# Optimization experiments

Hardware: AMD Instinct MI355X
Metric: run time of the kernel (lower is better)

Reference implementation:

```python
import jax, jax.numpy as jnp
import numpy as np

N = 100000   # nodes
E = 1250000  # edges
G = 64       # graphs in batch
F_IN, H, NT, GT = 29, 64, 6, 4
L = 4        # num GCN layers


def setup_inputs() -> dict:
    key = jax.random.key(0)
    ks = jax.random.split(key, 14)
    s_in = 1.0 / np.sqrt(F_IN)
    s_h = 1.0 / np.sqrt(H)
    return {
        "x": jax.random.normal(ks[0], (N, F_IN), dtype=jnp.float32),
        "edge_index": jax.random.randint(ks[1], (2, E), 0, N, dtype=jnp.int64),
        "batch": jnp.sort(jax.random.randint(ks[2], (N,), 0, G, dtype=jnp.int64)),
        "encW": jax.random.uniform(ks[3], (F_IN, H), jnp.float32, -s_in, s_in),
        "encb": jax.random.uniform(ks[4], (H,), jnp.float32, -s_in, s_in),
        "convW": jax.random.uniform(ks[5], (L, H, H), jnp.float32, -s_h, s_h),
        "convb": jax.random.uniform(ks[6], (L, H), jnp.float32, -s_h, s_h),
        "nodeW": jax.random.uniform(ks[7], (H, NT), jnp.float32, -s_h, s_h),
        "nodeb": jax.random.uniform(ks[8], (NT,), jnp.float32, -s_h, s_h),
        "g1W": jax.random.uniform(ks[9], (H, H), jnp.float32, -s_h, s_h),
        "g1b": jax.random.uniform(ks[10], (H,), jnp.float32, -s_h, s_h),
        "g2W": jax.random.uniform(ks[11], (H, GT), jnp.float32, -s_h, s_h),
        "g2b": jax.random.uniform(ks[12], (GT,), jnp.float32, -s_h, s_h),
    }


def reference(x, edge_index, batch, encW, encb, convW, convb, nodeW, nodeb, g1W, g1b, g2W, g2b):
    # GCNConv with self-loops and symmetric normalization (PyG defaults)
    loop = jnp.arange(N, dtype=edge_index.dtype)
    row = jnp.concatenate([edge_index[0], loop])  # senders
    col = jnp.concatenate([edge_index[1], loop])  # receivers
    deg = jax.ops.segment_sum(jnp.ones_like(col, dtype=x.dtype), col, num_segments=N)
    dis = jnp.where(deg > 0, deg ** -0.5, 0.0)
    norm = (dis[row] * dis[col])[:, None]  # [E+N, 1]

    h = jax.nn.relu(x @ encW + encb)
    for i in range(L):
        hw = h @ convW[i]  # transform then propagate
        agg = jax.ops.segment_sum(hw[row] * norm, col, num_segments=N)
        h = jax.nn.relu(agg + convb[i])

    pred_node = h @ nodeW + nodeb

    counts = jax.ops.segment_sum(jnp.ones((N,), x.dtype), batch, num_segments=G)
    gemb = jax.ops.segment_sum(h, batch, num_segments=G) / jnp.maximum(counts, 1.0)[:, None]
    pred_global = jax.nn.relu(gemb @ g1W + g1b) @ g2W + g2b
    return (pred_node, pred_global)
```

## Files before the change

### kernel.cpp

```cpp
#include <hip/hip_runtime.h>
#include <hip/hip_fp16.h>

#define N_NODES 100000
#define N_EDGES 1250000
#define N_GRAPHS 64
#define F_INN 29
#define HD 64
#define NT 6
#define GT 4
#define NLAYERS 4
#define RECS_CAP 3000000
#define NBLK 1563
#define NBUK 782
#define HGRID 256
#define GB_BLOCKS 391
#define ENC_BLOCKS 6250
#define NH_BLOCKS 3125

typedef __attribute__((ext_vector_type(8))) _Float16 f16x8;
typedef __attribute__((ext_vector_type(4))) float f32x4;

__global__ void hist1_misc(const int* __restrict__ col, int* __restrict__ ghistT, int E,
                           const float* __restrict__ convW, uint4* __restrict__ wfrag,
                           __half* __restrict__ ht1, __half* __restrict__ ht2,
                           const int* __restrict__ batch, int* __restrict__ start) {
    __shared__ int lh[NBUK];
    int tid = threadIdx.x, b = blockIdx.x;
    if (b < HGRID) {
        for (int i = tid; i < NBUK; i += 256) lh[i] = 0;
        __syncthreads();
        for (int e = b * 256 + tid; e < E; e += HGRID * 256) atomicAdd(&lh[col[e] >> 7], 1);
        __syncthreads();
        for (int i = tid; i < NBUK; i += 256) ghistT[i * 256 + b] = lh[i];
    } else if (b < HGRID + 4) {
        int layer = b - HGRID;
        const float* W = convW + (size_t)layer * HD * HD;
        uint4* out = wfrag + (size_t)layer * 512;
        for (int s = tid; s < 512; s += 256) {
            int jt = s >> 7, ks = (s >> 6) & 1, l = s & 63;
            int j = jt * 16 + (l & 15);
            int k0 = ks * 32 + (l >> 4) * 8;
            __align__(16) __half hh[8];
            #pragma unroll
            for (int i = 0; i < 8; ++i) hh[i] = __float2half_rn(W[(size_t)(k0 + i) * HD + j]);
            out[s] = *reinterpret_cast<const uint4*>(hh);
        }
    } else if (b == HGRID + 4) {
        if (tid < HD) ht1[(size_t)N_NODES * HD + tid] = __float2half_rn(0.f);
        else if (tid < 2 * HD) ht2[(size_t)N_NODES * HD + (tid - HD)] = __float2half_rn(0.f);
    } else {
        int i = (b - HGRID - 5) * 256 + tid;
        if (i < N_NODES) {
            int bb = batch[i];
            if (i == 0) {
                for (int g = 0; g <= bb; ++g) start[g] = 0;
            } else {
                int pb = batch[i - 1];
                if (pb != bb) for (int g = pb + 1; g <= bb; ++g) start[g] = i;
            }
            if (i == N_NODES - 1) {
                for (int g = bb + 1; g <= N_GRAPHS; ++g) start[g] = N_NODES;
            }
        }
    }
}

__global__ void hist_colscan(int* __restrict__ ghistT, int* __restrict__ tot) {
    __shared__ int wsum[4];
    int k = blockIdx.x, tid = threadIdx.x;
    int v = ghistT[k * 256 + tid];
    int incl = v;
    int lane = tid & 63;
    #pragma unroll
    for (int off = 1; off < 64; off <<= 1) {
        int t = __shfl_up(incl, (unsigned)off, 64);
        if (lane >= off) incl += t;
    }
    if (lane == 63) wsum[tid >> 6] = incl;
    __syncthreads();
    int woff = 0;
    for (int w = 0; w < (tid >> 6); ++w) woff += wsum[w];
    ghistT[k * 256 + tid] = woff + incl - v;
    if (tid == 255) tot[k] = woff + incl;
}

__global__ void scatter_buckets(const int* __restrict__ row, const int* __restrict__ col,
                                const int* __restrict__ ghistT, const int* __restrict__ tot,
                                int* __restrict__ boff,
                                unsigned* __restrict__ bke, int E) {
    __shared__ int boffL[NBUK];
    __shared__ int cur[NBUK];
    __shared__ int wsum[4];
    int tid = threadIdx.x, b = blockIdx.x;
    {
        int base = tid * 4;
        int v0 = (base + 0 < NBUK) ? tot[base + 0] : 0;
        int v1 = (base + 1 < NBUK) ? tot[base + 1] : 0;
        int v2 = (base + 2 < NBUK) ? tot[base + 2] : 0;
        int v3 = (base + 3 < NBUK) ? tot[base + 3] : 0;
        int tsum = v0 + v1 + v2 + v3;
        int incl = tsum;
        int lane = tid & 63;
        #pragma unroll
        for (int off = 1; off < 64; off <<= 1) {
            int t = __shfl_up(incl, (unsigned)off, 64);
            if (lane >= off) incl += t;
        }
        if (lane == 63) wsum[tid >> 6] = incl;
        __syncthreads();
        int woff = 0;
        for (int w = 0; w < (tid >> 6); ++w) woff += wsum[w];
        int run = woff + incl - tsum;
        if (base + 0 < NBUK) boffL[base + 0] = run; run += v0;
        if (base + 1 < NBUK) boffL[base + 1] = run; run += v1;
        if (base + 2 < NBUK) boffL[base + 2] = run; run += v2;
        if (base + 3 < NBUK) boffL[base + 3] = run;
    }
    __syncthreads();
    for (int i = tid; i < NBUK; i += 256) {
        cur[i] = ghistT[i * 256 + b] + boffL[i];
        if (b == 0) boff[i] = boffL[i];
    }
    __syncthreads();
    for (int e = b * 256 + tid; e < E; e += HGRID * 256) {
        int c = col[e];
        int pos = atomicAdd(&cur[c >> 7], 1);
        bke[pos] = (unsigned)row[e] | ((unsigned)(c & 127) << 25);
    }
}

__global__ void bucket_count(const unsigned* __restrict__ bke, const int* __restrict__ boff,
                             int* __restrict__ cnt16, float* __restrict__ dis,
                             int* __restrict__ btot, int E) {
    __shared__ int lc[128];
    __shared__ int red[2];
    int k = blockIdx.x, tid = threadIdx.x;
    if (tid < 128) lc[tid] = 0;
    __syncthreads();
    int s = boff[k];
    int t = (k == NBUK - 1) ? E : boff[k + 1];
    for (int i = s + tid; i < t; i += 256) atomicAdd(&lc[bke[i] >> 25], 1);
    __syncthreads();
    int c16 = 0;
    if (tid < 128) {
        int node = k * 128 + tid;
        if (node < N_NODES) {
            int c = lc[tid];
            c16 = (c + 15) & ~15;
            cnt16[node] = c16;
            dis[node] = rsqrtf((float)(c + 1));
        }
        int sum = c16;
        #pragma unroll
        for (int off = 1; off < 64; off <<= 1) sum += __shfl_xor(sum, off, 64);
        if ((tid & 63) == 0) red[tid >> 6] = sum;
    }
    __syncthreads();
    if (tid == 0) btot[k] = red[0] + red[1];
}

__global__ void fill_enc(const unsigned* __restrict__ bke, const int* __restrict__ boff,
                         const int* __restrict__ btot, const int* __restrict__ cnt16,
                         int* __restrict__ offs, int* __restrict__ srcs, int E,
                         const float* __restrict__ x, const float* __restrict__ encW,
                         const float* __restrict__ encb, const float* __restrict__ dis,
                         __half* __restrict__ ht) {
    int tid = threadIdx.x;
    int b = blockIdx.x;
    if (b < NBUK) {
        __shared__ int offsL[128];
        __shared__ int cur[128];
        __shared__ int wtot[2];
        __shared__ int wred[4];
        int k = b;
        int partial = 0;
        for (int i = tid; i < k; i += 256) partial += btot[i];
        {
            int lane = tid & 63;
            #pragma unroll
            for (int off = 1; off < 64; off <<= 1) partial += __shfl_xor(partial, off, 64);
            if (lane == 0) wred[tid >> 6] = partial;
        }
        __syncthreads();
        int bbasek = wred[0] + wred[1] + wred[2] + wred[3];
        int v = 0, incl = 0;
        if (tid < 128) {
            int node = k * 128 + tid;
            v = (node < N_NODES) ? cnt16[node] : 0;
            incl = v;
            int lane = tid & 63;
            #pragma unroll
            for (int off = 1; off < 64; off <<= 1) {
                int t = __shfl_up(incl, (unsigned)off, 64);
                if (lane >= off) incl += t;
            }
            if (lane == 63) wtot[tid >> 6] = incl;
        }
        __syncthreads();
        if (tid < 128) {
            int w0 = (tid >= 64) ? wtot[0] : 0;
            int node = k * 128 + tid;
            int o = bbasek + w0 + incl - v;
            offsL[tid] = o;
            cur[tid] = 0;
            if (node < N_NODES) offs[node] = o;
        }
        __syncthreads();
        int s = boff[k];
        int t = (k == NBUK - 1) ? E : boff[k + 1];
        for (int i = s + tid; i < t; i += 256) {
            unsigned u = bke[i];
            int l = u >> 25;
            int r = atomicAdd(&cur[l], 1);
            srcs[offsL[l] + r] = (int)(u & 0x01FFFFFFu);
        }
        __syncthreads();
        if (tid < 128) {
            int node = k * 128 + tid;
            if (node < N_NODES) {
                int c = cur[tid];
                int c16 = (c + 15) & ~15;
                int base = offsL[tid];
                for (int p = base + c; p < base + c16; ++p) srcs[p] = N_NODES;
            }
        }
    } else {
        __shared__ float Ws[F_INN * HD];
        __shared__ float bs[HD];
        __shared__ float xs[16 * F_INN];
        for (int i = tid; i < F_INN * HD; i += 256) Ws[i] = encW[i];
        if (tid < HD) bs[tid] = encb[tid];
        int n0 = (b - NBUK) * 16;
        for (int i = tid; i < 16 * F_INN; i += 256) {
            int nn = n0 + i / F_INN;
            xs[i] = (nn < N_NODES) ? x[(size_t)nn * F_INN + (i % F_INN)] : 0.f;
        }
        __syncthreads();
        #pragma unroll
        for (int it = 0; it < 4; ++it) {
            int l = it * 4 + (tid >> 6);
            int j = tid & 63;
            int nn = n0 + l;
            if (nn < N_NODES) {
                float a = bs[j];
                #pragma unroll
                for (int k = 0; k < F_INN; ++k) a = fmaf(xs[l * F_INN + k], Ws[k * HD + j], a);
                ht[(size_t)nn * HD + j] = __float2half_rn(dis[nn] * fmaxf(a, 0.f));
            }
        }
    }
}


#define H2(u) (*reinterpret_cast<const __half2*>(&(u)))
#define ROWQ(src) (*reinterpret_cast<const uint4*>(&ht[(size_t)(src) * HD + fh8]))
#define ACCQ(c, idx0, idx1) { \
    __half2 t0 = __hadd2(__hadd2(H2(r0.c), H2(r1.c)), __hadd2(H2(r2.c), H2(r3.c))); \
    __half2 t1 = __hadd2(__hadd2(H2(r4.c), H2(r5.c)), __hadd2(H2(r6.c), H2(r7.c))); \
    float2 f0 = __half22float2(t0); \
    float2 f1 = __half22float2(t1); \
    acc[idx0] += f0.x + f1.x; acc[idx1] += f0.y + f1.y; }

__global__ void layer_kernel(const __half* __restrict__ ht,
                             const int* __restrict__ offs, const int* __restrict__ cnt16,
                             const int4* __restrict__ srcs4,
                             const float* __restrict__ dis,
                             const uint4* __restrict__ wfragL, const float* __restrict__ bias,
                             __half* __restrict__ hout, int scaleOut) {
    __shared__ uint4 WfS[512];
    __shared__ __half aggS[64 * 72];
    __shared__ int offsS[64];
    __shared__ int cntS[64];
    __shared__ float disS[64];
    __shared__ float biasS[64];
    int tid = threadIdx.x;
    int b = blockIdx.x;
    WfS[tid] = wfragL[tid];
    WfS[tid + 256] = wfragL[tid + 256];
    if (tid < 64) {
        int d = b * 64 + tid;
        biasS[tid] = bias[tid];
        if (d < N_NODES) {
            offsS[tid] = offs[d];
            cntS[tid] = cnt16[d];
            disS[tid] = dis[d];
        } else {
            offsS[tid] = offs[N_NODES - 1] + cnt16[N_NODES - 1];
            cntS[tid] = 0;
            disS[tid] = 0.f;
        }
    }
    __syncthreads();

    int wave = tid >> 6;
    int lane = tid & 63;
    int q = lane >> 4;
    int lane16 = lane & 15;
    int sub = lane16 >> 3;
    int fh8 = (lane16 & 7) * 8;

    int l0 = wave * 16 + q * 4;
    {
        int nbase = b * 64 + l0;
        int d0 = sub * 2, d1 = sub * 2 + 1;
        *reinterpret_cast<uint4*>(&aggS[(l0 + d0) * 72 + fh8]) =
            *reinterpret_cast<const uint4*>(&ht[(size_t)min(nbase + d0, N_NODES) * HD + fh8]);
        *reinterpret_cast<uint4*>(&aggS[(l0 + d1) * 72 + fh8]) =
            *reinterpret_cast<const uint4*>(&ht[(size_t)min(nbase + d1, N_NODES) * HD + fh8]);
    }
    int s = offsS[l0];
    int e = offsS[l0 + 3] + cntS[l0 + 3];
    int dcur = l0;
    int nb = offsS[l0] + cntS[l0];
    float acc[8] = {0.f, 0.f, 0.f, 0.f, 0.f, 0.f, 0.f, 0.f};

    auto flush = [&](int d) {
        float a0 = acc[0] + __shfl_xor(acc[0], 8, 64);
        float a1 = acc[1] + __shfl_xor(acc[1], 8, 64);
        float a2 = acc[2] + __shfl_xor(acc[2], 8, 64);
        float a3 = acc[3] + __shfl_xor(acc[3], 8, 64);
        float a4 = acc[4] + __shfl_xor(acc[4], 8, 64);
        float a5 = acc[5] + __shfl_xor(acc[5], 8, 64);
        float a6 = acc[6] + __shfl_xor(acc[6], 8, 64);
        float a7 = acc[7] + __shfl_xor(acc[7], 8, 64);
        if (sub == 0) {
            uint4 sv = *reinterpret_cast<uint4*>(&aggS[d * 72 + fh8]);
            float2 s0 = __half22float2(H2(sv.x));
            float2 s1 = __half22float2(H2(sv.y));
            float2 s2 = __half22float2(H2(sv.z));
            float2 s3 = __half22float2(H2(sv.w));
            __half2 h0 = __floats2half2_rn(a0 + s0.x, a1 + s0.y);
            __half2 h1 = __floats2half2_rn(a2 + s1.x, a3 + s1.y);
            __half2 h2 = __floats2half2_rn(a4 + s2.x, a5 + s2.y);
            __half2 h3 = __floats2half2_rn(a6 + s3.x, a7 + s3.y);
            uint4 w;
            w.x = *(unsigned*)&h0;
            w.y = *(unsigned*)&h1;
            w.z = *(unsigned*)&h2;
            w.w = *(unsigned*)&h3;
            *reinterpret_cast<uint4*>(&aggS[d * 72 + fh8]) = w;
        }
        #pragma unroll
        for (int i = 0; i < 8; ++i) acc[i] = 0.f;
    };

    int4 i0, i1, i2, i3;
    if (s < e) {
        int base = s >> 2;
        i0 = srcs4[base + 0];
        i1 = srcs4[base + 1];
        i2 = srcs4[base + 2];
        i3 = srcs4[base + 3];
    }
    for (int p = s; p < e; p += 16) {
        int4 ia = sub ? i2 : i0;
        int4 ib = sub ? i3 : i1;
        uint4 r0 = ROWQ(ia.x), r1 = ROWQ(ia.y), r2 = ROWQ(ia.z), r3 = ROWQ(ia.w);
        uint4 r4 = ROWQ(ib.x), r5 = ROWQ(ib.y), r6 = ROWQ(ib.z), r7 = ROWQ(ib.w);
        int pn = p + 16;
        if (pn < e) {
            int base = pn >> 2;
            i0 = srcs4[base + 0];
            i1 = srcs4[base + 1];
            i2 = srcs4[base + 2];
            i3 = srcs4[base + 3];
        }
        while (p >= nb) {
            flush(dcur);
            ++dcur;
            nb = offsS[dcur] + cntS[dcur];
        }
        ACCQ(x, 0, 1);
        ACCQ(y, 2, 3);
        ACCQ(z, 4, 5);
        ACCQ(w, 6, 7);
    }
    while (dcur <= l0 + 3) {
        flush(dcur);
        ++dcur;
    }

    f32x4 c0 = {0.f, 0.f, 0.f, 0.f}, c1 = c0, c2 = c0, c3 = c0;
    #pragma unroll
    for (int ks = 0; ks < 2; ++ks) {
        f16x8 a = *reinterpret_cast<const f16x8*>(
            &aggS[(wave * 16 + (lane & 15)) * 72 + ks * 32 + (lane >> 4) * 8]);
        f16x8 b0 = *reinterpret_cast<const f16x8*>(&WfS[(0 * 2 + ks) * 64 + lane]);
        c0 = __builtin_amdgcn_mfma_f32_16x16x32_f16(a, b0, c0, 0, 0, 0);
        f16x8 b1 = *reinterpret_cast<const f16x8*>(&WfS[(1 * 2 + ks) * 64 + lane]);
        c1 = __builtin_amdgcn_mfma_f32_16x16x32_f16(a, b1, c1, 0, 0, 0);
        f16x8 b2 = *reinterpret_cast<const f16x8*>(&WfS[(2 * 2 + ks) * 64 + lane]);
        c2 = __builtin_amdgcn_mfma_f32_16x16x32_f16(a, b2, c2, 0, 0, 0);
        f16x8 b3 = *reinterpret_cast<const f16x8*>(&WfS[(3 * 2 + ks) * 64 + lane]);
        c3 = __builtin_amdgcn_mfma_f32_16x16x32_f16(a, b3, c3, 0, 0, 0);
    }
    #pragma unroll
    for (int jt = 0; jt < 4; ++jt) {
        f32x4 c = (jt == 0) ? c0 : (jt == 1) ? c1 : (jt == 2) ? c2 : c3;
        int j = jt * 16 + (lane & 15);
        float bj = biasS[j];
        #pragma unroll
        for (int i = 0; i < 4; ++i) {
            int rl = wave * 16 + (lane >> 4) * 4 + i;
            int node = b * 64 + rl;
            if (node < N_NODES) {
                float dn = disS[rl];
                float o = fmaxf(fmaf(dn, c[i], bj), 0.f);
                if (scaleOut) o *= dn;
                hout[(size_t)node * HD + j] = __float2half_rn(o);
            }
        }
    }
}

__global__ void heads_kernel(const __half* __restrict__ h, const float* __restrict__ W,
                             const float* __restrict__ bb, float* __restrict__ out,
                             const int* __restrict__ start, float* __restrict__ gpart) {
    int tid = threadIdx.x;
    int b = blockIdx.x;
    if (b < NH_BLOCKS) {
        __shared__ float Ws[HD * NT];
        __shared__ float bs[NT];
        __shared__ float hs[32 * 65];
        for (int i = tid; i < HD * NT; i += 256) Ws[i] = W[i];
        if (tid < NT) bs[tid] = bb[tid];
        int n0 = b * 32;
        const unsigned* hrow = reinterpret_cast<const unsigned*>(&h[(size_t)n0 * HD]);
        for (int i = tid; i < 32 * HD / 2; i += 256) {
            unsigned u = hrow[i];
            float2 f = __half22float2(*reinterpret_cast<const __half2*>(&u));
            int el = i * 2;
            int row = el >> 6, colc = el & 63;
            hs[row * 65 + colc] = f.x;
            hs[row * 65 + colc + 1] = f.y;
        }
        __syncthreads();
        int l = tid >> 3, t = tid & 7;
        int nn = n0 + l;
        if (nn < N_NODES && t < NT) {
            float a = bs[t];
            #pragma unroll
            for (int k = 0; k < HD; ++k) a = fmaf(hs[l * 65 + k], Ws[k * NT + t], a);
            out[(size_t)nn * NT + t] = a;
        }
    } else {
        __shared__ float red[4][HD];
        int pb = b - NH_BLOCKS;
        int g = pb >> 2, q = pb & 3;
        int s0 = start[g], e0 = start[g + 1];
        int len = e0 - s0;
        int qs = s0 + (len * q) / 4;
        int qe = s0 + (len * (q + 1)) / 4;
        int wave = tid >> 6, lane = tid & 63;
        float acc = 0.f;
        for (int r = qs + wave; r < qe; r += 4) acc += __half2float(h[(size_t)r * HD + lane]);
        red[wave][lane] = acc;
        __syncthreads();
        if (wave == 0)
            gpart[(size_t)pb * HD + lane] =
                red[0][lane] + red[1][lane] + red[2][lane] + red[3][lane];
    }
}

__global__ void global_head(const float* __restrict__ gpart, const int* __restrict__ start,
                            const float* __restrict__ g1W, const float* __restrict__ g1b,
                            const float* __restrict__ g2W, const float* __restrict__ g2b,
                            float* __restrict__ out) {
    __shared__ float rS[HD];
    int g = blockIdx.x;
    int j = threadIdx.x;
    int cnt = start[g + 1] - start[g];
    float inv = 1.f / fmaxf((float)cnt, 1.f);
    rS[j] = (gpart[(size_t)(4 * g + 0) * HD + j] + gpart[(size_t)(4 * g + 1) * HD + j] +
             gpart[(size_t)(4 * g + 2) * HD + j] + gpart[(size_t)(4 * g + 3) * HD + j]) * inv;
    __syncthreads();
    float a = g1b[j];
    #pragma unroll
    for (int k = 0; k < HD; ++k) a = fmaf(rS[k], g1W[k * HD + j], a);
    a = fmaxf(a, 0.f);
    float o0 = a * g2W[j * GT + 0];
    float o1 = a * g2W[j * GT + 1];
    float o2 = a * g2W[j * GT + 2];
    float o3 = a * g2W[j * GT + 3];
    #pragma unroll
    for (int off = 1; off < 64; off <<= 1) {
        o0 += __shfl_xor(o0, off, 64);
        o1 += __shfl_xor(o1, off, 64);
        o2 += __shfl_xor(o2, off, 64);
        o3 += __shfl_xor(o3, off, 64);
    }
    if (j == 0) {
        out[g * GT + 0] = o0 + g2b[0];
        out[g * GT + 1] = o1 + g2b[1];
        out[g * GT + 2] = o2 + g2b[2];
        out[g * GT + 3] = o3 + g2b[3];
    }
}


extern "C" void kernel_launch(void* const* d_in, const int* in_sizes, int n_in,
                              void* d_out, int out_size, void* d_ws, size_t ws_size,
                              hipStream_t stream) {
    const float* x    = (const float*)d_in[0];
    const int*   ei   = (const int*)d_in[1];
    const int*   batch= (const int*)d_in[2];
    const float* encW = (const float*)d_in[3];
    const float* encb = (const float*)d_in[4];
    const float* convW= (const float*)d_in[5];
    const float* convb= (const float*)d_in[6];
    const float* nodeW= (const float*)d_in[7];
    const float* nodeb= (const float*)d_in[8];
    const float* g1W  = (const float*)d_in[9];
    const float* g1b  = (const float*)d_in[10];
    const float* g2W  = (const float*)d_in[11];
    const float* g2b  = (const float*)d_in[12];
    float* out = (float*)d_out;

    const int N = N_NODES, E = N_EDGES;

    char* ws = (char*)d_ws;
    size_t off = 0;
    auto alloc = [&](size_t bytes) -> void* {
        void* p = ws + off;
        off += (bytes + 255) & ~(size_t)255;
        return p;
    };
    int*    ghistT = (int*)alloc((size_t)NBUK * 256 * 4);
    int*    tot    = (int*)alloc((size_t)NBUK * 4);
    int*    boff   = (int*)alloc((size_t)NBUK * 4);
    int*    btot   = (int*)alloc((size_t)NBUK * 4);
    unsigned* bke  = (unsigned*)alloc((size_t)E * 4);
    int*    offs   = (int*)alloc((size_t)N * 4);
    int*    cnt16  = (int*)alloc((size_t)N * 4);
    float*  dis    = (float*)alloc((size_t)N * 4);
    int*    start  = (int*)alloc((size_t)(N_GRAPHS + 1) * 4);
    float*  gpart  = (float*)alloc((size_t)N_GRAPHS * 4 * HD * 4);
    uint4*  wfrag  = (uint4*)alloc((size_t)NLAYERS * 512 * 16);
    int*    srcs   = (int*)alloc((size_t)RECS_CAP * 4);
    __half* ht1    = (__half*)alloc((size_t)(N + 1) * HD * 2);
    __half* ht2    = (__half*)alloc((size_t)(N + 1) * HD * 2);

    hist1_misc<<<HGRID + 5 + GB_BLOCKS, 256, 0, stream>>>(ei + E, ghistT, E, convW, wfrag,
                                                          ht1, ht2, batch, start);
    hist_colscan<<<NBUK, 256, 0, stream>>>(ghistT, tot);
    scatter_buckets<<<HGRID, 256, 0, stream>>>(ei, ei + E, ghistT, tot, boff, bke, E);
    bucket_count<<<NBUK, 256, 0, stream>>>(bke, boff, cnt16, dis, btot, E);
    fill_enc<<<NBUK + ENC_BLOCKS, 256, 0, stream>>>(bke, boff, btot, cnt16, offs, srcs, E,
                                                    x, encW, encb, dis, ht1);

    __half* hin = ht1;
    __half* hot = ht2;
    for (int i = 0; i < NLAYERS; ++i) {
        layer_kernel<<<NBLK, 256, 0, stream>>>(hin, offs, cnt16, (const int4*)srcs, dis,
                                               wfrag + (size_t)i * 512,
                                               convb + (size_t)i * HD,
                                               hot, (i < NLAYERS - 1) ? 1 : 0);
        __half* t = hin; hin = hot; hot = t;
    }

    heads_kernel<<<NH_BLOCKS + N_GRAPHS * 4, 256, 0, stream>>>(hin, nodeW, nodeb, out,
                                                               start, gpart);
    global_head<<<N_GRAPHS, 64, 0, stream>>>(gpart, start, g1W, g1b, g2W, g2b, out + (size_t)N * NT);
}
```

Baseline: 207.5 us.

## Balance per-quarter-wave edge work by sorting destinations by degree

Each 16-lane quarter of a wave used to process four consecutive destination nodes, so quarters with high-degree nodes ran long while the others idled. Now the 16 destinations of each wave are ranked by padded edge-chunk count and dealt out in snake order, so each quarter gets a similar total chunk count. The edge loop walks a per-quarter list of non-contiguous destinations and prefetches the next chunk across destination boundaries. This adds a shuffle-based ranking step, more branching in the loop, and less contiguous index reads.

```diff
diff --git a/kernel.cpp b/kernel.cpp
--- a/kernel.cpp
+++ b/kernel.cpp
@@ -273,6 +273,7 @@
     __shared__ int cntS[64];
     __shared__ float disS[64];
     __shared__ float biasS[64];
+    __shared__ int dqS[64];
     int tid = threadIdx.x;
     int b = blockIdx.x;
     WfS[tid] = wfragL[tid];
@@ -299,6 +300,26 @@
     int sub = lane16 >> 3;
     int fh8 = (lane16 & 7) * 8;
 
+    {
+        int g = cntS[wave * 16 + lane16] >> 4;
+        int rank = 0;
+        #pragma unroll
+        for (int k = 0; k < 16; ++k) {
+            int ok = __shfl(g, (lane & 48) | k, 64);
+            rank += (ok > g) || (ok == g && k < lane16);
+        }
+        if (lane < 16) {
+            int round = rank >> 2;
+            int pos = rank & 3;
+            int qq = (round & 1) ? (3 - pos) : pos;
+            dqS[wave * 16 + qq * 4 + round] = lane16;
+        }
+    }
+    int dlist0 = wave * 16 + dqS[wave * 16 + q * 4 + 0];
+    int dlist1 = wave * 16 + dqS[wave * 16 + q * 4 + 1];
+    int dlist2 = wave * 16 + dqS[wave * 16 + q * 4 + 2];
+    int dlist3 = wave * 16 + dqS[wave * 16 + q * 4 + 3];
+
     int l0 = wave * 16 + q * 4;
     {
         int nbase = b * 64 + l0;
@@ -308,10 +329,7 @@
         *reinterpret_cast<uint4*>(&aggS[(l0 + d1) * 72 + fh8]) =
             *reinterpret_cast<const uint4*>(&ht[(size_t)min(nbase + d1, N_NODES) * HD + fh8]);
     }
-    int s = offsS[l0];
-    int e = offsS[l0 + 3] + cntS[l0 + 3];
-    int dcur = l0;
-    int nb = offsS[l0] + cntS[l0];
+
     float acc[8] = {0.f, 0.f, 0.f, 0.f, 0.f, 0.f, 0.f, 0.f};
 
     auto flush = [&](int d) {
@@ -344,40 +362,70 @@
         for (int i = 0; i < 8; ++i) acc[i] = 0.f;
     };
 
+    auto destOf = [&](int t) -> int {
+        return (t == 0) ? dlist0 : (t == 1) ? dlist1 : (t == 2) ? dlist2 : dlist3;
+    };
+
+    int dsel = 0;
+    int dl = dlist0;
+    int p = offsS[dl];
+    int nb = p + cntS[dl];
+    while (dsel < 4 && p >= nb) {
+        flush(dl);
+        ++dsel;
+        if (dsel < 4) {
+            dl = destOf(dsel);
+            p = offsS[dl];
+            nb = p + cntS[dl];
+        }
+    }
     int4 i0, i1, i2, i3;
-    if (s < e) {
-        int base = s >> 2;
+    if (dsel < 4) {
+        int base = p >> 2;
         i0 = srcs4[base + 0];
         i1 = srcs4[base + 1];
         i2 = srcs4[base + 2];
         i3 = srcs4[base + 3];
     }
-    for (int p = s; p < e; p += 16) {
+    while (dsel < 4) {
         int4 ia = sub ? i2 : i0;
         int4 ib = sub ? i3 : i1;
         uint4 r0 = ROWQ(ia.x), r1 = ROWQ(ia.y), r2 = ROWQ(ia.z), r3 = ROWQ(ia.w);
         uint4 r4 = ROWQ(ib.x), r5 = ROWQ(ib.y), r6 = ROWQ(ib.z), r7 = ROWQ(ib.w);
-        int pn = p + 16;
-        if (pn < e) {
-            int base = pn >> 2;
-            i0 = srcs4[base + 0];
-            i1 = srcs4[base + 1];
-            i2 = srcs4[base + 2];
-            i3 = srcs4[base + 3];
-        }
-        while (p >= nb) {
-            flush(dcur);
-            ++dcur;
-            nb = offsS[dcur] + cntS[dcur];
+        {
+            int pn = p + 16;
+            int ds2 = dsel;
+            int nb2 = nb;
+            while (ds2 < 4 && pn >= nb2) {
+                ++ds2;
+                if (ds2 < 4) {
+                    int dl2 = destOf(ds2);
+                    pn = offsS[dl2];
+                    nb2 = pn + cntS[dl2];
+                }
+            }
+            if (ds2 < 4) {
+                int base = pn >> 2;
+                i0 = srcs4[base + 0];
+                i1 = srcs4[base + 1];
+                i2 = srcs4[base + 2];
+                i3 = srcs4[base + 3];
+            }
         }
         ACCQ(x, 0, 1);
         ACCQ(y, 2, 3);
         ACCQ(z, 4, 5);
         ACCQ(w, 6, 7);
-    }
-    while (dcur <= l0 + 3) {
-        flush(dcur);
-        ++dcur;
+        p += 16;
+        while (dsel < 4 && p >= nb) {
+            flush(dl);
+            ++dsel;
+            if (dsel < 4) {
+                dl = destOf(dsel);
+                p = offsS[dl];
+                nb = p + cntS[dl];
+            }
+        }
     }
 
     f32x4 c0 = {0.f, 0.f, 0.f, 0.f}, c1 = c0, c2 = c0, c3 = c0;
```

Result: slower. 213.2 us (+2.8%).
